# Performance work log

Measured on AMD Instinct MI355X. Metric: run time of the kernel, lower is better.

## Reference

```python
import jax, jax.numpy as jnp
import numpy as np

LATENT_DIM = 64
K = 128


def setup_inputs() -> dict:
    key = jax.random.key(0)
    ks = jax.random.split(key, 7)
    B, T, N, d, k = 64, 1024, 1024, LATENT_DIM, K
    return {
        "review_seq": jax.random.normal(ks[0], (B, T, d), dtype=jnp.float32),
        "post_seq": jax.random.normal(ks[1], (B, N, d), dtype=jnp.float32),
        "Wl": jax.random.normal(ks[2], (d, d), dtype=jnp.float32) * 0.05,
        "Wr": jax.random.normal(ks[3], (k, d), dtype=jnp.float32) * 0.05,
        "Wp": jax.random.normal(ks[4], (k, d), dtype=jnp.float32) * 0.05,
        "whr": jax.random.normal(ks[5], (1, k), dtype=jnp.float32) * 0.05,
        "whp": jax.random.normal(ks[6], (1, k), dtype=jnp.float32) * 0.05,
    }


def reference(review_seq, post_seq, Wl, Wr, Wp, whr, whp):
    # L[b,t,n] = tanh(review @ Wl @ post^T)
    L = jnp.tanh(jnp.einsum('btd,dD,bnD->btn', review_seq, Wl, post_seq))
    # Hp[b,k,n] = tanh(Wp @ post^T + Wr @ review^T @ L)
    Hp = jnp.tanh(jnp.einsum('kd,bnd->bkn', Wp, post_seq)
                  + jnp.einsum('kd,btd,btn->bkn', Wr, review_seq, L))
    # Hr[b,k,t] = tanh(Wr @ review^T + Wp @ post^T @ L^T)
    Hr = jnp.tanh(jnp.einsum('kd,btd->bkt', Wr, review_seq)
                  + jnp.einsum('kd,bnd,btn->bkt', Wp, post_seq, L))
    # attention weights over post (n) and review (t) positions
    Ap = jax.nn.softmax(jnp.einsum('yk,bkn->bn', whp, Hp), axis=-1)
    Ar = jax.nn.softmax(jnp.einsum('yk,bkt->bt', whr, Hr), axis=-1)
    co_p = jnp.einsum('bnd,bn->bd', post_seq, Ap)
    co_r = jnp.einsum('btd,bt->bd', review_seq, Ar)
    return jnp.concatenate([co_p, co_r], axis=1)  # [B, 2*latent_dim]
```

## Files before the change

kernel.cpp:

```cpp
#include <hip/hip_runtime.h>
#include <hip/hip_bf16.h>


typedef __attribute__((ext_vector_type(8))) short bfrag;
typedef __attribute__((ext_vector_type(4))) float ffrag;

__device__ __forceinline__ unsigned short f2b(float f) {
  unsigned u = __builtin_bit_cast(unsigned, f);
  u += 0x7FFFu + ((u >> 16) & 1u);
  return (unsigned short)(u >> 16);
}
__device__ __forceinline__ float b2f(unsigned short h) {
  return __builtin_bit_cast(float, (unsigned)h << 16);
}
__device__ __forceinline__ float ftanh(float x) {
  float e = __builtin_amdgcn_exp2f(x * 2.88539008177792681f);
  return fmaf(-2.0f, __builtin_amdgcn_rcpf(e + 1.0f), 1.0f);
}
__device__ __forceinline__ unsigned pack2(float lo, float hi) {
  unsigned a = __builtin_bit_cast(unsigned, lo) + 0x8000u;
  unsigned b = __builtin_bit_cast(unsigned, hi) + 0x8000u;
  return __builtin_amdgcn_perm(b, a, 0x07060302u);
}

#define MFMA(a, b, c) __builtin_amdgcn_mfma_f32_16x16x32_bf16((a), (b), (c), 0, 0, 0)

__global__ __launch_bounds__(256) void prep_kernel(
    const float* __restrict__ review, const float* __restrict__ post,
    const float* __restrict__ Wl, const float* __restrict__ Wr,
    const float* __restrict__ Wp,
    unsigned short* __restrict__ RWb, unsigned short* __restrict__ Rb,
    unsigned short* __restrict__ Pb, unsigned short* __restrict__ postb)
{
  const int chunk = blockIdx.x, b = blockIdx.y, side = blockIdx.z;
  const int tid = threadIdx.x, lane = tid & 63, w = tid >> 6;
  const int lr = lane & 15, lg = lane >> 4;
  const int r0 = chunk * 128;

  __shared__ __align__(16) unsigned short seqs[128][72];
  __shared__ __align__(16) unsigned short wgt[128][72];
  __shared__ __align__(16) unsigned short wlt[64][72];

  const float* seq = (side == 0) ? review : post;
  for (int i = tid; i < 128 * 64; i += 256) {
    int r = i >> 6, d = i & 63;
    unsigned short h = f2b(seq[((size_t)(b * 1024 + r0 + r)) * 64 + d]);
    seqs[r][d] = h;
    if (side == 1) postb[((size_t)(b * 1024 + r0 + r)) * 64 + d] = h;
  }
  const float* wkd = (side == 0) ? Wr : Wp;
  for (int i = tid; i < 128 * 64; i += 256) {
    int k = i >> 6, d = i & 63;
    wgt[k][d] = f2b(wkd[k * 64 + d]);
  }
  if (side == 0) {
    for (int i = tid; i < 64 * 64; i += 256) {
      int d = i >> 6, c = i & 63;
      wlt[c][d] = f2b(Wl[d * 64 + c]);
    }
  }
  __syncthreads();

  if (side == 0) {
    ffrag acc[2][4] = {};
#pragma unroll
    for (int ks = 0; ks < 2; ++ks)
#pragma unroll
      for (int ts = 0; ts < 2; ++ts) {
        bfrag a = *(const bfrag*)&seqs[w * 32 + ts * 16 + lr][ks * 32 + lg * 8];
#pragma unroll
        for (int is = 0; is < 4; ++is) {
          bfrag bb = *(const bfrag*)&wlt[is * 16 + lr][ks * 32 + lg * 8];
          acc[ts][is] = MFMA(a, bb, acc[ts][is]);
        }
      }
#pragma unroll
    for (int ts = 0; ts < 2; ++ts)
#pragma unroll
      for (int is = 0; is < 4; ++is)
#pragma unroll
        for (int j = 0; j < 4; ++j) {
          int t = r0 + w * 32 + ts * 16 + lg * 4 + j;
          int i2 = is * 16 + lr;
          RWb[((size_t)(b * 1024 + t)) * 64 + i2] = f2b(acc[ts][is][j]);
        }
  }
  {
    ffrag acc[2][8] = {};
#pragma unroll
    for (int ks = 0; ks < 2; ++ks)
#pragma unroll
      for (int ksb = 0; ksb < 2; ++ksb) {
        bfrag a = *(const bfrag*)&wgt[w * 32 + ksb * 16 + lr][ks * 32 + lg * 8];
#pragma unroll
        for (int ts = 0; ts < 8; ++ts) {
          bfrag bb = *(const bfrag*)&seqs[ts * 16 + lr][ks * 32 + lg * 8];
          acc[ksb][ts] = MFMA(a, bb, acc[ksb][ts]);
        }
      }
    unsigned short* dst = (side == 0) ? Rb : Pb;
#pragma unroll
    for (int ksb = 0; ksb < 2; ++ksb)
#pragma unroll
      for (int ts = 0; ts < 8; ++ts)
#pragma unroll
        for (int j = 0; j < 4; ++j) {
          int k = w * 32 + ksb * 16 + lg * 4 + j;
          int t = r0 + ts * 16 + lr;
          dst[((size_t)(b * 128 + k)) * 1024 + t] = f2b(acc[ksb][ts][j]);
        }
  }
}

__global__ __launch_bounds__(256, 4) void hz_kernel(
    const unsigned short* __restrict__ RWb, const unsigned short* __restrict__ Rb,
    const unsigned short* __restrict__ Pb, const unsigned short* __restrict__ postb,
    const float* __restrict__ whp, const float* __restrict__ whr,
    float* __restrict__ zp, float* __restrict__ zr)
{
  const int orig = blockIdx.x;
  const int swz = (orig & 7) * 128 + (orig >> 3);
  const int strip = swz & 7, pair = swz >> 3;
  const int b = pair & 63, role = pair >> 6;
  const int s0 = strip * 128;
  const int tid = threadIdx.x, lane = tid & 63, w = tid >> 6;
  const int lr = lane & 15, lg = lane >> 4;

  const unsigned short* resident = role ? RWb : postb;
  const unsigned short* chunkseq = role ? postb : RWb;
  const unsigned short* coeff    = role ? Pb : Rb;
  const unsigned short* addterm  = role ? Rb : Pb;
  const float* wh                = role ? whr : whp;
  float* zout                    = role ? zr : zp;

  __shared__ __align__(16) char smem[36864];
  char* postl = smem;
  char* rwl   = smem + 16384;
  char* rl    = smem + 20480;
  char* ll    = smem + 28672;
  float* zacc = (float*)(smem + 28672);

  {
    const char* src = (const char*)resident + ((size_t)(b * 1024 + s0)) * 128;
    const int row = tid >> 1, half = tid & 1;
#pragma unroll
    for (int q = 0; q < 4; ++q) {
      int slot = half * 4 + q;
      uint4 v = *(const uint4*)(src + row * 128 + slot * 16);
      *(uint4*)(postl + row * 128 + ((slot ^ (row & 7)) << 4)) = v;
    }
  }
  {
    const char* csrc = (const char*)chunkseq + ((size_t)(b * 1024)) * 128;
    const int r = tid >> 3, slot = tid & 7;
    uint4 v = *(const uint4*)(csrc + r * 128 + slot * 16);
    *(uint4*)(rwl + r * 128 + ((slot ^ (r & 7)) << 4)) = v;
    const char* ksrc = (const char*)coeff + ((size_t)(b * 128)) * 2048;
    const int k0 = tid >> 2, part = tid & 3;
    uint4 v0 = *(const uint4*)(ksrc + (size_t)k0 * 2048 + part * 16);
    uint4 v1 = *(const uint4*)(ksrc + (size_t)(k0 + 64) * 2048 + part * 16);
    *(uint4*)(rl + part * 2048 + k0 * 16) = v0;
    *(uint4*)(rl + part * 2048 + (k0 + 64) * 16) = v1;
  }
  __syncthreads();

  ffrag acc[2][8] = {};
  uint4 pf_c, pf_k0, pf_k1;
  const int pr = tid >> 3, pslot = tid & 7;
  const int pk = tid >> 2, ppart = tid & 3;

  for (int tc = 0; tc < 32; ++tc) {
    if (tc < 31) {
      const char* csrc = (const char*)chunkseq + ((size_t)(b * 1024 + (tc + 1) * 32)) * 128;
      pf_c = *(const uint4*)(csrc + pr * 128 + pslot * 16);
      const char* ksrc = (const char*)coeff + ((size_t)(b * 128)) * 2048 + (tc + 1) * 64;
      pf_k0 = *(const uint4*)(ksrc + (size_t)pk * 2048 + ppart * 16);
      pf_k1 = *(const uint4*)(ksrc + (size_t)(pk + 64) * 2048 + ppart * 16);
    }

    ffrag la[2][2] = {};
#pragma unroll
    for (int ks = 0; ks < 2; ++ks)
#pragma unroll
      for (int ts = 0; ts < 2; ++ts) {
        const int arow = ts * 16 + lr;
        bfrag a = *(const bfrag*)(rwl + arow * 128 + (((ks * 4 + lg) ^ (arow & 7)) << 4));
#pragma unroll
        for (int ns = 0; ns < 2; ++ns) {
          const int brow = w * 32 + ns * 16 + lr;
          bfrag bb = *(const bfrag*)(postl + brow * 128 + (((ks * 4 + lg) ^ (brow & 7)) << 4));
          la[ts][ns] = MFMA(a, bb, la[ts][ns]);
        }
      }
#pragma unroll
    for (int ts = 0; ts < 2; ++ts)
#pragma unroll
      for (int ns = 0; ns < 2; ++ns) {
        const int res = w * 32 + ns * 16 + lr;
        uint2 pkv;
        pkv.x = pack2(ftanh(la[ts][ns][0]), ftanh(la[ts][ns][1]));
        pkv.y = pack2(ftanh(la[ts][ns][2]), ftanh(la[ts][ns][3]));
        *(uint2*)(ll + (ts * 2 + (lg >> 1)) * 2048 + res * 16 + (lg & 1) * 8) = pkv;
      }
    __syncthreads();

    bfrag bbr[8];
#pragma unroll
    for (int ns = 0; ns < 8; ++ns)
      bbr[ns] = *(const bfrag*)(ll + lg * 2048 + (ns * 16 + lr) * 16);
#pragma unroll
    for (int ksb = 0; ksb < 2; ++ksb) {
      bfrag a = *(const bfrag*)(rl + lg * 2048 + (w * 32 + ksb * 16 + lr) * 16);
#pragma unroll
      for (int ns = 0; ns < 8; ++ns)
        acc[ksb][ns] = MFMA(a, bbr[ns], acc[ksb][ns]);
    }
    if (tc < 31)
      *(uint4*)(rwl + pr * 128 + ((pslot ^ (pr & 7)) << 4)) = pf_c;
    __syncthreads();
    if (tc < 31) {
      *(uint4*)(rl + ppart * 2048 + pk * 16) = pf_k0;
      *(uint4*)(rl + ppart * 2048 + (pk + 64) * 16) = pf_k1;
    }
  }

  float zpart[8] = {0, 0, 0, 0, 0, 0, 0, 0};
#pragma unroll
  for (int ksb = 0; ksb < 2; ++ksb)
#pragma unroll
    for (int j = 0; j < 4; ++j) {
      const int k = w * 32 + ksb * 16 + lg * 4 + j;
      const float whk = wh[k];
      const unsigned short* arow = addterm + ((size_t)(b * 128 + k)) * 1024 + s0;
#pragma unroll
      for (int ns = 0; ns < 8; ++ns) {
        const int res = ns * 16 + lr;
        float h = ftanh(acc[ksb][ns][j] + b2f(arow[res]));
        zpart[ns] += whk * h;
      }
    }
#pragma unroll
  for (int ns = 0; ns < 8; ++ns) {
    zpart[ns] += __shfl_xor(zpart[ns], 16);
    zpart[ns] += __shfl_xor(zpart[ns], 32);
  }
  if (lg == 0) {
#pragma unroll
    for (int ns = 0; ns < 8; ++ns) zacc[w * 128 + ns * 16 + lr] = zpart[ns];
  }
  __syncthreads();
  if (tid < 128)
    zout[(size_t)b * 1024 + s0 + tid] =
        zacc[tid] + zacc[128 + tid] + zacc[256 + tid] + zacc[384 + tid];
}

__global__ __launch_bounds__(256) void final_kernel(
    const float* __restrict__ review, const float* __restrict__ post,
    const float* __restrict__ zp, const float* __restrict__ zr,
    float* __restrict__ out)
{
  const int b = blockIdx.x, side = blockIdx.y, tid = threadIdx.x;
  __shared__ float zl[1024];
  __shared__ float red[256];
  __shared__ float cacc[4][64];

  const float* z = (side == 0) ? zp : zr;
  const float* seq = (side == 0) ? post : review;
  for (int i = tid; i < 1024; i += 256) zl[i] = z[(size_t)b * 1024 + i];
  __syncthreads();
  float m = -3.4e38f;
  for (int i = tid; i < 1024; i += 256) m = fmaxf(m, zl[i]);
  red[tid] = m;
  __syncthreads();
  for (int s = 128; s > 0; s >>= 1) {
    if (tid < s) red[tid] = fmaxf(red[tid], red[tid + s]);
    __syncthreads();
  }
  m = red[0];
  __syncthreads();
  float sm = 0.f;
  for (int i = tid; i < 1024; i += 256) {
    float e = __expf(zl[i] - m);
    zl[i] = e;
    sm += e;
  }
  red[tid] = sm;
  __syncthreads();
  for (int s = 128; s > 0; s >>= 1) {
    if (tid < s) red[tid] += red[tid + s];
    __syncthreads();
  }
  float inv = 1.0f / red[0];
  __syncthreads();
  const int d = tid & 63, g = tid >> 6;
  float a = 0.f;
  for (int n = g * 256; n < g * 256 + 256; ++n)
    a += zl[n] * seq[((size_t)(b * 1024 + n)) * 64 + d];
  cacc[g][d] = a * inv;
  __syncthreads();
  if (tid < 64)
    out[b * 128 + side * 64 + tid] =
        cacc[0][tid] + cacc[1][tid] + cacc[2][tid] + cacc[3][tid];
}

extern "C" void kernel_launch(void* const* d_in, const int* in_sizes, int n_in,
                              void* d_out, int out_size, void* d_ws, size_t ws_size,
                              hipStream_t stream) {
  const float* review = (const float*)d_in[0];
  const float* post   = (const float*)d_in[1];
  const float* Wl     = (const float*)d_in[2];
  const float* Wr     = (const float*)d_in[3];
  const float* Wp     = (const float*)d_in[4];
  const float* whr    = (const float*)d_in[5];
  const float* whp    = (const float*)d_in[6];
  float* out = (float*)d_out;

  char* ws = (char*)d_ws;
  unsigned short* RWb   = (unsigned short*)(ws);
  unsigned short* Rb    = (unsigned short*)(ws + (size_t)8  * 1048576);
  unsigned short* Pb    = (unsigned short*)(ws + (size_t)24 * 1048576);
  unsigned short* postb = (unsigned short*)(ws + (size_t)40 * 1048576);
  float* zp = (float*)(ws + (size_t)48 * 1048576);
  float* zr = (float*)(ws + (size_t)48 * 1048576 + 262144);

  prep_kernel<<<dim3(8, 64, 2), dim3(256), 0, stream>>>(
      review, post, Wl, Wr, Wp, RWb, Rb, Pb, postb);
  hz_kernel<<<dim3(1024), dim3(256), 0, stream>>>(
      RWb, Rb, Pb, postb, whp, whr, zp, zr);
  final_kernel<<<dim3(64, 2), dim3(256), 0, stream>>>(
      review, post, zp, zr, out);
}
```

Before: 108.7 us.

## Load MFMA fragments directly to registers, double-buffer L, widen final softmax kernel

The hz kernel now loads the chunk-sequence and coefficient fragments from global memory straight into registers with a software prefetch instead of staging them through LDS. The tanh(L) tile is double-buffered so the next chunk's L is computed while the current one is consumed, which removes one barrier per iteration and shrinks LDS use. The final kernel uses 1024 threads with wave-shuffle reductions in place of tree reductions through shared memory. In exchange the fragment loads go uncoalesced straight to registers, and register pressure rises.

```diff
diff --git a/kernel.cpp b/kernel.cpp
--- a/kernel.cpp
+++ b/kernel.cpp
@@ -133,12 +133,25 @@
   const float* wh                = role ? whr : whp;
   float* zout                    = role ? zr : zp;
 
-  __shared__ __align__(16) char smem[36864];
+  __shared__ __align__(16) char smem[32768];
   char* postl = smem;
-  char* rwl   = smem + 16384;
-  char* rl    = smem + 20480;
-  char* ll    = smem + 28672;
-  float* zacc = (float*)(smem + 28672);
+  char* ll0   = smem + 16384;
+  char* ll1   = smem + 24576;
+  float* zacc = (float*)(smem + 16384);
+
+  const char* cbase = (const char*)chunkseq + (size_t)b * 131072
+                      + (size_t)lr * 128 + lg * 16;
+  const char* kbase = (const char*)coeff + (size_t)b * 262144
+                      + (size_t)(w * 32 + lr) * 2048 + lg * 16;
+
+  bfrag cfU[4], kfU[2];
+#pragma unroll
+  for (int ts = 0; ts < 2; ++ts)
+#pragma unroll
+    for (int ks = 0; ks < 2; ++ks)
+      cfU[ts * 2 + ks] = *(const bfrag*)(cbase + ts * 2048 + ks * 64);
+  kfU[0] = *(const bfrag*)(kbase);
+  kfU[1] = *(const bfrag*)(kbase + 32768);
 
   {
     const char* src = (const char*)resident + ((size_t)(b * 1024 + s0)) * 128;
@@ -150,48 +163,25 @@
       *(uint4*)(postl + row * 128 + ((slot ^ (row & 7)) << 4)) = v;
     }
   }
+  __syncthreads();
+
   {
-    const char* csrc = (const char*)chunkseq + ((size_t)(b * 1024)) * 128;
-    const int r = tid >> 3, slot = tid & 7;
-    uint4 v = *(const uint4*)(csrc + r * 128 + slot * 16);
-    *(uint4*)(rwl + r * 128 + ((slot ^ (r & 7)) << 4)) = v;
-    const char* ksrc = (const char*)coeff + ((size_t)(b * 128)) * 2048;
-    const int k0 = tid >> 2, part = tid & 3;
-    uint4 v0 = *(const uint4*)(ksrc + (size_t)k0 * 2048 + part * 16);
-    uint4 v1 = *(const uint4*)(ksrc + (size_t)(k0 + 64) * 2048 + part * 16);
-    *(uint4*)(rl + part * 2048 + k0 * 16) = v0;
-    *(uint4*)(rl + part * 2048 + (k0 + 64) * 16) = v1;
-  }
-  __syncthreads();
-
-  ffrag acc[2][8] = {};
-  uint4 pf_c, pf_k0, pf_k1;
-  const int pr = tid >> 3, pslot = tid & 7;
-  const int pk = tid >> 2, ppart = tid & 3;
-
-  for (int tc = 0; tc < 32; ++tc) {
-    if (tc < 31) {
-      const char* csrc = (const char*)chunkseq + ((size_t)(b * 1024 + (tc + 1) * 32)) * 128;
-      pf_c = *(const uint4*)(csrc + pr * 128 + pslot * 16);
-      const char* ksrc = (const char*)coeff + ((size_t)(b * 128)) * 2048 + (tc + 1) * 64;
-      pf_k0 = *(const uint4*)(ksrc + (size_t)pk * 2048 + ppart * 16);
-      pf_k1 = *(const uint4*)(ksrc + (size_t)(pk + 64) * 2048 + ppart * 16);
-    }
-
+    bfrag bb[2][2];
+#pragma unroll
+    for (int ks = 0; ks < 2; ++ks)
+#pragma unroll
+      for (int ns = 0; ns < 2; ++ns) {
+        const int brow = w * 32 + ns * 16 + lr;
+        bb[ks][ns] = *(const bfrag*)(postl + brow * 128 + (((ks * 4 + lg) ^ (brow & 7)) << 4));
+      }
     ffrag la[2][2] = {};
 #pragma unroll
     for (int ks = 0; ks < 2; ++ks)
 #pragma unroll
-      for (int ts = 0; ts < 2; ++ts) {
-        const int arow = ts * 16 + lr;
-        bfrag a = *(const bfrag*)(rwl + arow * 128 + (((ks * 4 + lg) ^ (arow & 7)) << 4));
-#pragma unroll
-        for (int ns = 0; ns < 2; ++ns) {
-          const int brow = w * 32 + ns * 16 + lr;
-          bfrag bb = *(const bfrag*)(postl + brow * 128 + (((ks * 4 + lg) ^ (brow & 7)) << 4));
-          la[ts][ns] = MFMA(a, bb, la[ts][ns]);
-        }
-      }
+      for (int ts = 0; ts < 2; ++ts)
+#pragma unroll
+        for (int ns = 0; ns < 2; ++ns)
+          la[ts][ns] = MFMA(cfU[ts * 2 + ks], bb[ks][ns], la[ts][ns]);
 #pragma unroll
     for (int ts = 0; ts < 2; ++ts)
 #pragma unroll
@@ -200,28 +190,76 @@
         uint2 pkv;
         pkv.x = pack2(ftanh(la[ts][ns][0]), ftanh(la[ts][ns][1]));
         pkv.y = pack2(ftanh(la[ts][ns][2]), ftanh(la[ts][ns][3]));
-        *(uint2*)(ll + (ts * 2 + (lg >> 1)) * 2048 + res * 16 + (lg & 1) * 8) = pkv;
-      }
+        *(uint2*)(ll0 + (ts * 2 + (lg >> 1)) * 2048 + res * 16 + (lg & 1) * 8) = pkv;
+      }
+  }
+#pragma unroll
+  for (int ts = 0; ts < 2; ++ts)
+#pragma unroll
+    for (int ks = 0; ks < 2; ++ks)
+      cfU[ts * 2 + ks] = *(const bfrag*)(cbase + 4096 + ts * 2048 + ks * 64);
+  __syncthreads();
+
+  ffrag acc[2][8] = {};
+  char* llc = ll0;
+  char* lln = ll1;
+
+#pragma unroll 2
+  for (int tc = 0; tc < 32; ++tc) {
+    if (tc < 31) {
+      bfrag bb[2][2];
+#pragma unroll
+      for (int ks = 0; ks < 2; ++ks)
+#pragma unroll
+        for (int ns = 0; ns < 2; ++ns) {
+          const int brow = w * 32 + ns * 16 + lr;
+          bb[ks][ns] = *(const bfrag*)(postl + brow * 128 + (((ks * 4 + lg) ^ (brow & 7)) << 4));
+        }
+      ffrag la[2][2] = {};
+#pragma unroll
+      for (int ks = 0; ks < 2; ++ks)
+#pragma unroll
+        for (int ts = 0; ts < 2; ++ts)
+#pragma unroll
+          for (int ns = 0; ns < 2; ++ns)
+            la[ts][ns] = MFMA(cfU[ts * 2 + ks], bb[ks][ns], la[ts][ns]);
+#pragma unroll
+      for (int ts = 0; ts < 2; ++ts)
+#pragma unroll
+        for (int ns = 0; ns < 2; ++ns) {
+          const int res = w * 32 + ns * 16 + lr;
+          uint2 pkv;
+          pkv.x = pack2(ftanh(la[ts][ns][0]), ftanh(la[ts][ns][1]));
+          pkv.y = pack2(ftanh(la[ts][ns][2]), ftanh(la[ts][ns][3]));
+          *(uint2*)(lln + (ts * 2 + (lg >> 1)) * 2048 + res * 16 + (lg & 1) * 8) = pkv;
+        }
+    }
+
+    {
+      const int tc2 = (tc + 2 <= 31) ? tc + 2 : 31;
+      const int tk  = (tc + 1 <= 31) ? tc + 1 : 31;
+      const char* c2 = cbase + (size_t)tc2 * 4096;
+#pragma unroll
+      for (int ts = 0; ts < 2; ++ts)
+#pragma unroll
+        for (int ks = 0; ks < 2; ++ks)
+          cfU[ts * 2 + ks] = *(const bfrag*)(c2 + ts * 2048 + ks * 64);
+      const char* k2 = kbase + (size_t)tk * 64;
+      bfrag nk0 = *(const bfrag*)(k2);
+      bfrag nk1 = *(const bfrag*)(k2 + 32768);
+
+#pragma unroll
+      for (int ns = 0; ns < 8; ++ns) {
+        bfrag bbr = *(const bfrag*)(llc + lg * 2048 + (ns * 16 + lr) * 16);
+        acc[0][ns] = MFMA(kfU[0], bbr, acc[0][ns]);
+        acc[1][ns] = MFMA(kfU[1], bbr, acc[1][ns]);
+      }
+      kfU[0] = nk0;
+      kfU[1] = nk1;
+    }
+
+    { char* t = llc; llc = lln; lln = t; }
     __syncthreads();
-
-    bfrag bbr[8];
-#pragma unroll
-    for (int ns = 0; ns < 8; ++ns)
-      bbr[ns] = *(const bfrag*)(ll + lg * 2048 + (ns * 16 + lr) * 16);
-#pragma unroll
-    for (int ksb = 0; ksb < 2; ++ksb) {
-      bfrag a = *(const bfrag*)(rl + lg * 2048 + (w * 32 + ksb * 16 + lr) * 16);
-#pragma unroll
-      for (int ns = 0; ns < 8; ++ns)
-        acc[ksb][ns] = MFMA(a, bbr[ns], acc[ksb][ns]);
-    }
-    if (tc < 31)
-      *(uint4*)(rwl + pr * 128 + ((pslot ^ (pr & 7)) << 4)) = pf_c;
-    __syncthreads();
-    if (tc < 31) {
-      *(uint4*)(rl + ppart * 2048 + pk * 16) = pf_k0;
-      *(uint4*)(rl + ppart * 2048 + (pk + 64) * 16) = pf_k1;
-    }
   }
 
   float zpart[8] = {0, 0, 0, 0, 0, 0, 0, 0};
@@ -254,53 +292,56 @@
         zacc[tid] + zacc[128 + tid] + zacc[256 + tid] + zacc[384 + tid];
 }
 
-__global__ __launch_bounds__(256) void final_kernel(
+__global__ __launch_bounds__(1024) void final_kernel(
     const float* __restrict__ review, const float* __restrict__ post,
     const float* __restrict__ zp, const float* __restrict__ zr,
     float* __restrict__ out)
 {
   const int b = blockIdx.x, side = blockIdx.y, tid = threadIdx.x;
+  const int wid = tid >> 6, lane = tid & 63;
   __shared__ float zl[1024];
-  __shared__ float red[256];
-  __shared__ float cacc[4][64];
+  __shared__ float red[16];
+  __shared__ float cacc[16][64];
 
   const float* z = (side == 0) ? zp : zr;
   const float* seq = (side == 0) ? post : review;
-  for (int i = tid; i < 1024; i += 256) zl[i] = z[(size_t)b * 1024 + i];
-  __syncthreads();
-  float m = -3.4e38f;
-  for (int i = tid; i < 1024; i += 256) m = fmaxf(m, zl[i]);
-  red[tid] = m;
-  __syncthreads();
-  for (int s = 128; s > 0; s >>= 1) {
-    if (tid < s) red[tid] = fmaxf(red[tid], red[tid + s]);
-    __syncthreads();
-  }
+
+  float v = z[(size_t)b * 1024 + tid];
+  zl[tid] = v;
+  float m = v;
+#pragma unroll
+  for (int off = 32; off; off >>= 1) m = fmaxf(m, __shfl_xor(m, off));
+  if (lane == 0) red[wid] = m;
+  __syncthreads();
   m = red[0];
-  __syncthreads();
-  float sm = 0.f;
-  for (int i = tid; i < 1024; i += 256) {
-    float e = __expf(zl[i] - m);
-    zl[i] = e;
-    sm += e;
-  }
-  red[tid] = sm;
-  __syncthreads();
-  for (int s = 128; s > 0; s >>= 1) {
-    if (tid < s) red[tid] += red[tid + s];
-    __syncthreads();
-  }
-  float inv = 1.0f / red[0];
-  __syncthreads();
-  const int d = tid & 63, g = tid >> 6;
+#pragma unroll
+  for (int i = 1; i < 16; ++i) m = fmaxf(m, red[i]);
+  __syncthreads();
+
+  float e = __expf(v - m);
+  zl[tid] = e;
+  float sm = e;
+#pragma unroll
+  for (int off = 32; off; off >>= 1) sm += __shfl_xor(sm, off);
+  if (lane == 0) red[wid] = sm;
+  __syncthreads();
+  sm = red[0];
+#pragma unroll
+  for (int i = 1; i < 16; ++i) sm += red[i];
+  const float inv = 1.0f / sm;
+
+  const int d = lane;
   float a = 0.f;
-  for (int n = g * 256; n < g * 256 + 256; ++n)
+  for (int n = wid * 64; n < wid * 64 + 64; ++n)
     a += zl[n] * seq[((size_t)(b * 1024 + n)) * 64 + d];
-  cacc[g][d] = a * inv;
-  __syncthreads();
-  if (tid < 64)
-    out[b * 128 + side * 64 + tid] =
-        cacc[0][tid] + cacc[1][tid] + cacc[2][tid] + cacc[3][tid];
+  cacc[wid][d] = a;
+  __syncthreads();
+  if (tid < 64) {
+    float s = 0.f;
+#pragma unroll
+    for (int g = 0; g < 16; ++g) s += cacc[g][tid];
+    out[b * 128 + side * 64 + tid] = s * inv;
+  }
 }
 
 extern "C" void kernel_launch(void* const* d_in, const int* in_sizes, int n_in,
@@ -327,6 +368,6 @@
       review, post, Wl, Wr, Wp, RWb, Rb, Pb, postb);
   hz_kernel<<<dim3(1024), dim3(256), 0, stream>>>(
       RWb, Rb, Pb, postb, whp, whr, zp, zr);
-  final_kernel<<<dim3(64, 2), dim3(256), 0, stream>>>(
+  final_kernel<<<dim3(64, 2), dim3(1024), 0, stream>>>(
       review, post, zp, zr, out);
 }
```

Result: slower. 138.8 us (+27.7%).
